# Optimization experiments

Measured on AMD Instinct MI355X. Metric: run time of the kernel, lower is better.

The kernel has to match this reference:

```python
import jax, jax.numpy as jnp
import numpy as np
from jax import lax

Q = 0.707  # torchaudio default Q for lowpass/highpass_biquad

def _shift(x, k):
    # delay along time axis by k samples, zero-padded (zero initial conditions)
    pad = jnp.zeros(x.shape[:-1] + (k,), x.dtype)
    return jnp.concatenate([pad, x[..., :-k]], axis=-1)

def _iir2(ff, a1, a2):
    # y[n] = ff[n] - a1*y[n-1] - a2*y[n-2], zero init state; scan over time
    ff_t = jnp.moveaxis(ff, -1, 0)              # [T, B, C]
    y0 = jnp.zeros(ff.shape[:-1], ff.dtype)     # [B, C]
    def step(carry, f):
        y1, y2 = carry
        y = f - a1 * y1 - a2 * y2
        return (y, y1), y
    _, y = lax.scan(step, (y0, y0), ff_t)
    return jnp.moveaxis(y, 0, -1)

def _biquad(x, b0, b1, b2, a0, a1, a2):
    # torchaudio.functional.biquad: normalize all coeffs by a0, then lfilter
    b0, b1, b2 = b0 / a0, b1 / a0, b2 / a0
    a1, a2 = a1 / a0, a2 / a0
    ff = b0 * x + b1 * _shift(x, 1) + b2 * _shift(x, 2)  # FIR part, vectorized
    return _iir2(ff, a1, a2)

def _lowpass_biquad(x, sr, cutoff):
    w0 = 2.0 * jnp.pi * cutoff / sr
    cos_w0 = jnp.cos(w0)
    alpha = jnp.sin(w0) / (2.0 * Q)
    b0 = (1.0 - cos_w0) / 2.0
    b1 = 1.0 - cos_w0
    b2 = b0
    a0 = 1.0 + alpha
    a1 = -2.0 * cos_w0
    a2 = 1.0 - alpha
    return _biquad(x, b0, b1, b2, a0, a1, a2)

def _highpass_biquad(x, sr, cutoff):
    w0 = 2.0 * jnp.pi * cutoff / sr
    cos_w0 = jnp.cos(w0)
    alpha = jnp.sin(w0) / (2.0 * Q)
    b0 = (1.0 + cos_w0) / 2.0
    b1 = -(1.0 + cos_w0)
    b2 = b0
    a0 = 1.0 + alpha
    a1 = -2.0 * cos_w0
    a2 = 1.0 - alpha
    return _biquad(x, b0, b1, b2, a0, a1, a2)

def setup_inputs() -> dict:
    key = jax.random.key(0)
    k1, = jax.random.split(key, 1)
    audio = jax.random.normal(k1, (32, 2, 220500), dtype=jnp.float32) * 0.1
    return {
        "audio": audio,
        "sample_rate": 44100,
        "cutoff_low": jnp.float32(200.0),
        "cutoff_high": jnp.float32(5000.0),
    }

def reference(audio, sample_rate, cutoff_low, cutoff_high):
    sr = jnp.float32(sample_rate)
    audio_low = _lowpass_biquad(audio, sr, cutoff_low)
    audio_high = _highpass_biquad(audio, sr, cutoff_high)
    return audio_low - audio_high
```

## Files before the change

### kernel.cpp

```cpp
#include <hip/hip_runtime.h>
#include <math.h>

#define T_LEN  220500
#define SEG    64
#define TPB    64
#define WARML  8
#define WOUT   ((64 - WARML) * SEG)
#define WSLOTS (WOUT / 4)
#define NWIN   ((T_LEN + WOUT - 1) / WOUT)

__device__ __forceinline__ int swz(int s) { return s ^ ((s >> 4) & 7); }

__global__ __launch_bounds__(TPB) void bandpass_kernel(
    const float* __restrict__ x,
    const int* __restrict__ sr_p,
    const float* __restrict__ fl_p,
    const float* __restrict__ fh_p,
    float* __restrict__ out)
{
    __shared__ float4 lds4[WSLOTS];

    const int lane = threadIdx.x;
    const int win  = blockIdx.x;
    const int seq  = blockIdx.y;

    const float sr   = (float)sr_p[0];
    const float twoQ = (float)(2.0 * 0.707);

    float w0 = (float)(2.0 * M_PI) * fl_p[0] / sr;
    float cw = cosf(w0);
    float al = sinf(w0) / twoQ;
    float a0 = 1.0f + al;
    const float lb0  = (1.0f - cw) * 0.5f / a0;
    const float lb1  = (1.0f - cw) / a0;
    const float lb2  = lb0;
    const float lna1 = 2.0f * cw / a0;
    const float lna2 = -(1.0f - al) / a0;

    w0 = (float)(2.0 * M_PI) * fh_p[0] / sr;
    cw = cosf(w0);
    al = sinf(w0) / twoQ;
    a0 = 1.0f + al;
    const float hb0  = (1.0f + cw) * 0.5f / a0;
    const float hb1  = -(1.0f + cw) / a0;
    const float hb2  = hb0;
    const float hna1 = 2.0f * cw / a0;
    const float hna2 = -(1.0f - al) / a0;

    const float* __restrict__ xs = x   + (size_t)seq * T_LEN;
    float*       __restrict__ os = out + (size_t)seq * T_LEN;

    const int Wbase = win * WOUT;
    const int s0    = Wbase - WARML * SEG + lane * SEG;

    float4 xr[16];
#pragma unroll
    for (int i = 0; i < 16; ++i) {
        const int g  = s0 + 4 * i;
        const int gc = min(max(g, 0), T_LEN - 4);
        float4 v = *(const float4*)(xs + gc);
        if (g < 0 || g >= T_LEN) v = make_float4(0.f, 0.f, 0.f, 0.f);
        xr[i] = v;
    }

    float xh1 = __shfl_up(xr[15].w, 1, 64);
    float xh2 = __shfl_up(xr[15].z, 1, 64);
    if (lane == 0) {
        xh1 = (s0 >= 1) ? xs[s0 - 1] : 0.f;
        xh2 = (s0 >= 2) ? xs[s0 - 2] : 0.f;
    }

    float x1 = xh1, x2 = xh2;
    float ly1 = 0.f, ly2 = 0.f, hy1 = 0.f, hy2 = 0.f;
#pragma unroll
    for (int i = 0; i < 16; ++i) {
        const float xa[4] = {xr[i].x, xr[i].y, xr[i].z, xr[i].w};
#pragma unroll
        for (int k = 0; k < 4; ++k) {
            const float xc  = xa[k];
            const float ffl = fmaf(lb0, xc, fmaf(lb1, x1, lb2 * x2));
            const float yl  = fmaf(lna2, ly2, fmaf(lna1, ly1, ffl));
            const float ffh = fmaf(hb0, xc, fmaf(hb1, x1, hb2 * x2));
            const float yh  = fmaf(hna2, hy2, fmaf(hna1, hy1, ffh));
            ly2 = ly1; ly1 = yl; hy2 = hy1; hy1 = yh;
            x2 = x1; x1 = xc;
        }
    }

    float la = lna1, lb = lna2, lc = 1.0f, ld = 0.0f;
    float ha = hna1, hb = hna2, hc = 1.0f, hd = 0.0f;
#pragma unroll
    for (int i = 0; i < 6; ++i) {
        float t0 = fmaf(la, la, lb * lc), t1 = fmaf(la, lb, lb * ld);
        float t2 = fmaf(lc, la, ld * lc), t3 = fmaf(lc, lb, ld * ld);
        la = t0; lb = t1; lc = t2; ld = t3;
        t0 = fmaf(ha, ha, hb * hc); t1 = fmaf(ha, hb, hb * hd);
        t2 = fmaf(hc, ha, hd * hc); t3 = fmaf(hc, hb, hd * hd);
        ha = t0; hb = t1; hc = t2; hd = t3;
    }

    float4 p = make_float4(ly1, ly2, hy1, hy2);
#pragma unroll
    for (int k = 0; k < 4; ++k) {
        const int d = 1 << k;
        float qx = __shfl_up(p.x, d, 64);
        float qy = __shfl_up(p.y, d, 64);
        float qz = __shfl_up(p.z, d, 64);
        float qw = __shfl_up(p.w, d, 64);
        if (lane < d) { qx = 0.f; qy = 0.f; qz = 0.f; qw = 0.f; }
        p.x = fmaf(la, qx, fmaf(lb, qy, p.x));
        p.y = fmaf(lc, qx, fmaf(ld, qy, p.y));
        p.z = fmaf(ha, qz, fmaf(hb, qw, p.z));
        p.w = fmaf(hc, qz, fmaf(hd, qw, p.w));
        float t0 = fmaf(la, la, lb * lc), t1 = fmaf(la, lb, lb * ld);
        float t2 = fmaf(lc, la, ld * lc), t3 = fmaf(lc, lb, ld * ld);
        la = t0; lb = t1; lc = t2; ld = t3;
        t0 = fmaf(ha, ha, hb * hc); t1 = fmaf(ha, hb, hb * hd);
        t2 = fmaf(hc, ha, hd * hc); t3 = fmaf(hc, hb, hd * hd);
        ha = t0; hb = t1; hc = t2; hd = t3;
    }
    float sx0 = __shfl_up(p.x, 1, 64);
    float sx1 = __shfl_up(p.y, 1, 64);
    float sx2 = __shfl_up(p.z, 1, 64);
    float sx3 = __shfl_up(p.w, 1, 64);
    if (lane == 0) { sx0 = 0.f; sx1 = 0.f; sx2 = 0.f; sx3 = 0.f; }

    if (lane >= WARML) {
        float bx1 = xh1, bx2 = xh2;
        float Ly1 = sx0, Ly2 = sx1, Hy1 = sx2, Hy2 = sx3;
        const int sb = (lane - WARML) * 16;
#pragma unroll
        for (int i = 0; i < 16; ++i) {
            const float xa[4] = {xr[i].x, xr[i].y, xr[i].z, xr[i].w};
            float o[4];
#pragma unroll
            for (int k = 0; k < 4; ++k) {
                const float xc  = xa[k];
                const float ffl = fmaf(lb0, xc, fmaf(lb1, bx1, lb2 * bx2));
                const float yl  = fmaf(lna2, Ly2, fmaf(lna1, Ly1, ffl));
                const float ffh = fmaf(hb0, xc, fmaf(hb1, bx1, hb2 * bx2));
                const float yh  = fmaf(hna2, Hy2, fmaf(hna1, Hy1, ffh));
                Ly2 = Ly1; Ly1 = yl; Hy2 = Hy1; Hy1 = yh;
                bx2 = bx1; bx1 = xc;
                o[k] = yl - yh;
            }
            lds4[swz(sb + i)] = make_float4(o[0], o[1], o[2], o[3]);
        }
    }

    __syncthreads();

#pragma unroll
    for (int k = 0; k < WSLOTS / 64; ++k) {
        const int slot = 64 * k + lane;
        const float4 v = lds4[swz(slot)];
        const int g = Wbase + 4 * slot;
        if (g < T_LEN) *(float4*)(os + g) = v;
    }
}

extern "C" void kernel_launch(void* const* d_in, const int* in_sizes, int n_in,
                              void* d_out, int out_size, void* d_ws, size_t ws_size,
                              hipStream_t stream) {
    const float* x  = (const float*)d_in[0];
    const int*   sr = (const int*)d_in[1];
    const float* fl = (const float*)d_in[2];
    const float* fh = (const float*)d_in[3];
    float* outp = (float*)d_out;

    const int nseq = in_sizes[0] / T_LEN;

    dim3 block(TPB);
    dim3 grid(NWIN, nseq);
    hipLaunchKernelGGL(bandpass_kernel, grid, block, 0, stream,
                       x, sr, fl, fh, outp);
}
```

Baseline: 118.4 us.

## Stage input through LDS with direct global-to-LDS loads and halve segment length

```diff
diff --git a/kernel.cpp b/kernel.cpp
--- a/kernel.cpp
+++ b/kernel.cpp
@@ -1,27 +1,39 @@
 #include <hip/hip_runtime.h>
 #include <math.h>
+#include <stdint.h>
 
 #define T_LEN  220500
-#define SEG    64
-#define TPB    64
-#define WARML  8
+#define SEG    32
+#define TPB    128
+#define WARML  16
 #define WOUT   ((64 - WARML) * SEG)
-#define WSLOTS (WOUT / 4)
+#define RS4    512
 #define NWIN   ((T_LEN + WOUT - 1) / WOUT)
+#define NBX    (NWIN / 2)
 
-__device__ __forceinline__ int swz(int s) { return s ^ ((s >> 4) & 7); }
+__device__ __forceinline__ int swz(int s) { return s ^ ((s >> 3) & 7); }
+
+__device__ __forceinline__ void glds16(const float* src, float4* dst_lds) {
+    __builtin_amdgcn_global_load_lds(
+        (const __attribute__((address_space(1))) void*)src,
+        (__attribute__((address_space(3))) void*)dst_lds,
+        16, 0, 0);
+}
 
 __global__ __launch_bounds__(TPB) void bandpass_kernel(
     const float* __restrict__ x,
     const int* __restrict__ sr_p,
     const float* __restrict__ fl_p,
     const float* __restrict__ fh_p,
-    float* __restrict__ out)
+    float* __restrict__ out,
+    const float* __restrict__ zbuf)
 {
-    __shared__ float4 lds4[WSLOTS];
+    __shared__ float4 lds4[2][RS4];
 
-    const int lane = threadIdx.x;
-    const int win  = blockIdx.x;
+    const int tid  = threadIdx.x;
+    const int lane = tid & 63;
+    const int wv   = tid >> 6;
+    const int win  = blockIdx.x * 2 + wv;
     const int seq  = blockIdx.y;
 
     const float sr   = (float)sr_p[0];
@@ -51,29 +63,37 @@
     float*       __restrict__ os = out + (size_t)seq * T_LEN;
 
     const int Wbase = win * WOUT;
-    const int s0    = Wbase - WARML * SEG + lane * SEG;
+    const int G0    = Wbase - WARML * SEG;
 
-    float4 xr[16];
+    float4* ldsw = lds4[wv];
+
 #pragma unroll
-    for (int i = 0; i < 16; ++i) {
-        const int g  = s0 + 4 * i;
-        const int gc = min(max(g, 0), T_LEN - 4);
-        float4 v = *(const float4*)(xs + gc);
-        if (g < 0 || g >= T_LEN) v = make_float4(0.f, 0.f, 0.f, 0.f);
-        xr[i] = v;
+    for (int k = 0; k < 8; ++k) {
+        const int jsrc = 64 * k + (lane ^ ((lane >> 3) & 7));
+        const int g    = G0 + 4 * jsrc;
+        const float* src = (g >= 0 && g + 4 <= T_LEN) ? (xs + g) : zbuf;
+        glds16(src, &ldsw[64 * k]);
+    }
+    __syncthreads();
+
+    float xh1, xh2;
+    if (lane > 0) {
+        const float4 h = ldsw[swz(8 * lane - 1)];
+        xh1 = h.w; xh2 = h.z;
+    } else {
+        xh1 = (G0 >= 1) ? xs[G0 - 1] : 0.f;
+        xh2 = (G0 >= 2) ? xs[G0 - 2] : 0.f;
     }
 
-    float xh1 = __shfl_up(xr[15].w, 1, 64);
-    float xh2 = __shfl_up(xr[15].z, 1, 64);
-    if (lane == 0) {
-        xh1 = (s0 >= 1) ? xs[s0 - 1] : 0.f;
-        xh2 = (s0 >= 2) ? xs[s0 - 2] : 0.f;
-    }
+    const int b = 8 * lane;
+    float4 xr[8];
+#pragma unroll
+    for (int i = 0; i < 8; ++i) xr[i] = ldsw[swz(b + i)];
 
     float x1 = xh1, x2 = xh2;
     float ly1 = 0.f, ly2 = 0.f, hy1 = 0.f, hy2 = 0.f;
 #pragma unroll
-    for (int i = 0; i < 16; ++i) {
+    for (int i = 0; i < 8; ++i) {
         const float xa[4] = {xr[i].x, xr[i].y, xr[i].z, xr[i].w};
 #pragma unroll
         for (int k = 0; k < 4; ++k) {
@@ -90,7 +110,7 @@
     float la = lna1, lb = lna2, lc = 1.0f, ld = 0.0f;
     float ha = hna1, hb = hna2, hc = 1.0f, hd = 0.0f;
 #pragma unroll
-    for (int i = 0; i < 6; ++i) {
+    for (int i = 0; i < 5; ++i) {
         float t0 = fmaf(la, la, lb * lc), t1 = fmaf(la, lb, lb * ld);
         float t2 = fmaf(lc, la, ld * lc), t3 = fmaf(lc, lb, ld * ld);
         la = t0; lb = t1; lc = t2; ld = t3;
@@ -101,7 +121,7 @@
 
     float4 p = make_float4(ly1, ly2, hy1, hy2);
 #pragma unroll
-    for (int k = 0; k < 4; ++k) {
+    for (int k = 0; k < 5; ++k) {
         const int d = 1 << k;
         float qx = __shfl_up(p.x, d, 64);
         float qy = __shfl_up(p.y, d, 64);
@@ -128,9 +148,8 @@
     if (lane >= WARML) {
         float bx1 = xh1, bx2 = xh2;
         float Ly1 = sx0, Ly2 = sx1, Hy1 = sx2, Hy2 = sx3;
-        const int sb = (lane - WARML) * 16;
 #pragma unroll
-        for (int i = 0; i < 16; ++i) {
+        for (int i = 0; i < 8; ++i) {
             const float xa[4] = {xr[i].x, xr[i].y, xr[i].z, xr[i].w};
             float o[4];
 #pragma unroll
@@ -144,18 +163,16 @@
                 bx2 = bx1; bx1 = xc;
                 o[k] = yl - yh;
             }
-            lds4[swz(sb + i)] = make_float4(o[0], o[1], o[2], o[3]);
+            ldsw[swz(b + i)] = make_float4(o[0], o[1], o[2], o[3]);
         }
     }
-
     __syncthreads();
 
 #pragma unroll
-    for (int k = 0; k < WSLOTS / 64; ++k) {
-        const int slot = 64 * k + lane;
-        const float4 v = lds4[swz(slot)];
-        const int g = Wbase + 4 * slot;
-        if (g < T_LEN) *(float4*)(os + g) = v;
+    for (int k = 0; k < 6; ++k) {
+        const int slot = 128 + 64 * k + lane;
+        const int g = Wbase + 4 * (64 * k + lane);
+        if (g < T_LEN) *(float4*)(os + g) = ldsw[swz(slot)];
     }
 }
 
@@ -168,10 +185,12 @@
     const float* fh = (const float*)d_in[3];
     float* outp = (float*)d_out;
 
+    hipMemsetAsync(d_ws, 0, 256, stream);
+
     const int nseq = in_sizes[0] / T_LEN;
 
     dim3 block(TPB);
-    dim3 grid(NWIN, nseq);
+    dim3 grid(NBX, nseq);
     hipLaunchKernelGGL(bandpass_kernel, grid, block, 0, stream,
-                       x, sr, fl, fh, outp);
+                       x, sr, fl, fh, outp, (const float*)d_ws);
 }
```

Result: faster. 116.0 us (-2.0%).
